# Kernel tuning notes

Hardware: AMD Instinct MI355X
Metric: run time of the kernel (lower is better)

## Reference

```python
import jax, jax.numpy as jnp
import numpy as np

D_MODEL = 1024
NUM_HEADS = 16
D_K = D_MODEL // NUM_HEADS


def setup_inputs() -> dict:
    key = jax.random.key(0)
    ks = jax.random.split(key, 11)
    B, S = 2, 2048
    scale = 1.0 / np.sqrt(D_MODEL)
    inp = {
        "q": jax.random.normal(ks[0], (B, S, D_MODEL), jnp.float32),
        "k": jax.random.normal(ks[1], (B, S, D_MODEL), jnp.float32),
        "v": jax.random.normal(ks[2], (B, S, D_MODEL), jnp.float32),
        "wq_w": jax.random.normal(ks[3], (D_MODEL, D_MODEL), jnp.float32) * scale,
        "wq_b": jnp.zeros((D_MODEL,), jnp.float32),
        "wk_w": jax.random.normal(ks[4], (D_MODEL, D_MODEL), jnp.float32) * scale,
        "wk_b": jnp.zeros((D_MODEL,), jnp.float32),
        "wv_w": jax.random.normal(ks[5], (D_MODEL, D_MODEL), jnp.float32) * scale,
        "wv_b": jnp.zeros((D_MODEL,), jnp.float32),
        "wo_w": jax.random.normal(ks[6], (D_MODEL, D_MODEL), jnp.float32) * scale,
        "wo_b": jnp.zeros((D_MODEL,), jnp.float32),
    }
    return inp


def reference(q, k, v, wq_w, wq_b, wk_w, wk_b, wv_w, wv_b, wo_w, wo_b):
    B, S, _ = q.shape
    H, dk = NUM_HEADS, D_K
    # projections (torch Linear: x @ W.T + b); reshape to [B, H, S, dk]
    qh = (q @ wq_w.T + wq_b).reshape(B, S, H, dk).transpose(0, 2, 1, 3)
    kh = (k @ wk_w.T + wk_b).reshape(B, S, H, dk).transpose(0, 2, 1, 3)
    vh = (v @ wv_w.T + wv_b).reshape(B, S, H, dk).transpose(0, 2, 1, 3)
    # explicit [B,H,S,S] scores, softmax over keys
    scores = jnp.einsum('bhqd,bhkd->bhqk', qh, kh) / np.sqrt(dk).astype(jnp.float32)
    weights = jax.nn.softmax(scores, axis=-1)
    out = jnp.einsum('bhqk,bhkd->bhqd', weights, vh)
    out = out.transpose(0, 2, 1, 3).reshape(B, S, H * dk)
    return out @ wo_w.T + wo_b
```

## Files before the change

kernel.cpp:

```cpp
#include <hip/hip_runtime.h>

#define B_  2
#define S_  2048
#define D_  1024
#define H_  16
#define DK_ 64

typedef __bf16 bf16;
typedef __bf16 bf16x8 __attribute__((ext_vector_type(8)));
typedef __bf16 bf16x4 __attribute__((ext_vector_type(4)));
typedef float  f32x4  __attribute__((ext_vector_type(4)));

#define GLD16(gptr, lptr) __builtin_amdgcn_global_load_lds( \
    (const __attribute__((address_space(1))) void*)(gptr),  \
    (__attribute__((address_space(3))) void*)(lptr), 16, 0, 0)

__global__ __launch_bounds__(256) void cast_all(
    const float* __restrict__ q, const float* __restrict__ k, const float* __restrict__ v,
    const float* __restrict__ wq, const float* __restrict__ wk, const float* __restrict__ wv,
    const float* __restrict__ wo,
    bf16* __restrict__ qb, bf16* __restrict__ kb, bf16* __restrict__ vb,
    bf16* __restrict__ wqb, bf16* __restrict__ wkb, bf16* __restrict__ wvb,
    bf16* __restrict__ wob) {
  int blk = blockIdx.x;
  const float* in; bf16* out; int base;
  if      (blk < 2048) { in = q;  out = qb;  base = blk; }
  else if (blk < 4096) { in = k;  out = kb;  base = blk - 2048; }
  else if (blk < 6144) { in = v;  out = vb;  base = blk - 4096; }
  else if (blk < 6656) { in = wq; out = wqb; base = blk - 6144; }
  else if (blk < 7168) { in = wk; out = wkb; base = blk - 6656; }
  else if (blk < 7680) { in = wv; out = wvb; base = blk - 7168; }
  else                 { in = wo; out = wob; base = blk - 7680; }
  int i = (base * 256 + threadIdx.x) * 8;
  float4 a = *(const float4*)(in + i);
  float4 b = *(const float4*)(in + i + 4);
  bf16x8 o;
  o[0] = (bf16)a.x; o[1] = (bf16)a.y; o[2] = (bf16)a.z; o[3] = (bf16)a.w;
  o[4] = (bf16)b.x; o[5] = (bf16)b.y; o[6] = (bf16)b.z; o[7] = (bf16)b.w;
  *(bf16x8*)(out + i) = o;
}

__global__ __launch_bounds__(256, 6) void gemm_qkv(
    const bf16* __restrict__ qb, const bf16* __restrict__ kb, const bf16* __restrict__ vb,
    const bf16* __restrict__ wq, const bf16* __restrict__ wk, const bf16* __restrict__ wv,
    const float* __restrict__ biq, const float* __restrict__ bik, const float* __restrict__ biv,
    bf16* __restrict__ Qh, bf16* __restrict__ Kh, bf16* __restrict__ Vt) {
  __shared__ bf16 As[128 * 64];
  __shared__ bf16 Bs[64 * 64];
  const int z = blockIdx.y;
  const bf16 *A, *Bm; const float* bias; bf16* Cout;
  int bx, by, N;
  if (z == 0)      { A = qb; Bm = wq; bias = biq; Cout = Qh; }
  else if (z == 1) { A = kb; Bm = wk; bias = bik; Cout = Kh; }
  else             { A = wv; Bm = vb; bias = biv; Cout = Vt; }
  if (z < 2) { by = blockIdx.x & 31; bx = blockIdx.x >> 5; N = D_; }
  else       { bx = blockIdx.x & 63; by = blockIdx.x >> 6; N = B_ * S_; }
  const int K = D_;

  const int tid  = threadIdx.x;
  const int wave = tid >> 6, lane = tid & 63;
  const int g = lane >> 4, r = lane & 15;
  const int m0 = by * 128, n0 = bx * 64;

  f32x4 acc[2][4] = {};
  const int srow = tid >> 3;
  const int sp   = tid & 7;

  for (int k0 = 0; k0 < K; k0 += 64) {
    __syncthreads();
#pragma unroll
    for (int rep = 0; rep < 4; rep++) {
      int row = rep * 32 + srow;
      int bb  = sp ^ (row & 7);
      GLD16(A + (size_t)(m0 + row) * K + k0 + bb * 8, As + rep * 2048 + wave * 512);
    }
#pragma unroll
    for (int rep = 0; rep < 2; rep++) {
      int row = rep * 32 + srow;
      int bb  = sp ^ (row & 7);
      GLD16(Bm + (size_t)(n0 + row) * K + k0 + bb * 8, Bs + rep * 2048 + wave * 512);
    }
    __syncthreads();

#pragma unroll
    for (int kc = 0; kc < 2; kc++) {
      bf16x8 af[2], bfr[4];
#pragma unroll
      for (int i = 0; i < 2; i++) {
        int row = wave * 32 + i * 16 + r;
        af[i] = *(const bf16x8*)(As + row * 64 + (((kc * 4 + g) ^ (row & 7)) * 8));
      }
#pragma unroll
      for (int j = 0; j < 4; j++) {
        int row = j * 16 + r;
        bfr[j] = *(const bf16x8*)(Bs + row * 64 + (((kc * 4 + g) ^ (row & 7)) * 8));
      }
#pragma unroll
      for (int i = 0; i < 2; i++)
#pragma unroll
        for (int j = 0; j < 4; j++)
          acc[i][j] = __builtin_amdgcn_mfma_f32_16x16x32_bf16(af[i], bfr[j], acc[i][j], 0, 0, 0);
    }
  }

  const float qscale = 0.18033688f;
#pragma unroll
  for (int i = 0; i < 2; i++) {
#pragma unroll
    for (int j = 0; j < 4; j++) {
#pragma unroll
      for (int t = 0; t < 4; t++) {
        int mrow = m0 + wave * 32 + i * 16 + g * 4 + t;
        int col  = n0 + j * 16 + r;
        float val = acc[i][j][t];
        if (z < 2) {
          val += bias[col];
          if (z == 0) val *= qscale;
          int bb2 = mrow >> 11, s = mrow & (S_ - 1);
          int hh = col >> 6, d = col & 63;
          Cout[(((size_t)(bb2 * H_ + hh)) * S_ + s) * 64 + d] = (bf16)val;
        } else {
          val += bias[mrow];
          Cout[(size_t)mrow * N + col] = (bf16)val;
        }
      }
    }
  }
}

__global__ __launch_bounds__(256, 6) void gemm_out(const bf16* __restrict__ A,
                                                   const bf16* __restrict__ Bm,
                                                   const float* __restrict__ bias,
                                                   float* __restrict__ Cout) {
  __shared__ bf16 As[128 * 64];
  __shared__ bf16 Bs[64 * 64];
  const int K = D_, N = D_;
  const int tid  = threadIdx.x;
  const int wave = tid >> 6, lane = tid & 63;
  const int g = lane >> 4, r = lane & 15;
  const int bx = blockIdx.x & 15, by = blockIdx.x >> 4;
  const int m0 = by * 128, n0 = bx * 64;

  f32x4 acc[2][4] = {};
  const int srow = tid >> 3;
  const int sp   = tid & 7;

  for (int k0 = 0; k0 < K; k0 += 64) {
    __syncthreads();
#pragma unroll
    for (int rep = 0; rep < 4; rep++) {
      int row = rep * 32 + srow;
      int bb  = sp ^ (row & 7);
      GLD16(A + (size_t)(m0 + row) * K + k0 + bb * 8, As + rep * 2048 + wave * 512);
    }
#pragma unroll
    for (int rep = 0; rep < 2; rep++) {
      int row = rep * 32 + srow;
      int bb  = sp ^ (row & 7);
      GLD16(Bm + (size_t)(n0 + row) * K + k0 + bb * 8, Bs + rep * 2048 + wave * 512);
    }
    __syncthreads();

#pragma unroll
    for (int kc = 0; kc < 2; kc++) {
      bf16x8 af[2], bfr[4];
#pragma unroll
      for (int i = 0; i < 2; i++) {
        int row = wave * 32 + i * 16 + r;
        af[i] = *(const bf16x8*)(As + row * 64 + (((kc * 4 + g) ^ (row & 7)) * 8));
      }
#pragma unroll
      for (int j = 0; j < 4; j++) {
        int row = j * 16 + r;
        bfr[j] = *(const bf16x8*)(Bs + row * 64 + (((kc * 4 + g) ^ (row & 7)) * 8));
      }
#pragma unroll
      for (int i = 0; i < 2; i++)
#pragma unroll
        for (int j = 0; j < 4; j++)
          acc[i][j] = __builtin_amdgcn_mfma_f32_16x16x32_bf16(af[i], bfr[j], acc[i][j], 0, 0, 0);
    }
  }

#pragma unroll
  for (int i = 0; i < 2; i++)
#pragma unroll
    for (int j = 0; j < 4; j++)
#pragma unroll
      for (int t = 0; t < 4; t++) {
        int mrow = m0 + wave * 32 + i * 16 + g * 4 + t;
        int col  = n0 + j * 16 + r;
        Cout[(size_t)mrow * N + col] = acc[i][j][t] + bias[col];
      }
}

__global__ __launch_bounds__(256, 4) void flash_attn(const bf16* __restrict__ Qh,
                                                     const bf16* __restrict__ Kh,
                                                     const bf16* __restrict__ Vt,
                                                     bf16* __restrict__ Apart,
                                                     float* __restrict__ Lpart) {
  __shared__ bf16 Ks[64 * 64];
  __shared__ bf16 Vs[64 * 64];
  __shared__ bf16 Ps[128 * 40];

  const int tid  = threadIdx.x;
  const int wave = tid >> 6, lane = tid & 63;
  const int g = lane >> 4, r = lane & 15;

  int qt = blockIdx.x >> 6;
  int kh = blockIdx.x & 1;
  int bh = (blockIdx.x >> 1) & 31;
  int h = bh & (H_ - 1), b = bh >> 4;

  const bf16* Kbase = Kh + ((size_t)bh * S_ + kh * 1024) * DK_;
  const bf16* Vbase = Vt + (size_t)h * 64 * (B_ * S_) + (size_t)b * S_ + kh * 1024;

  bf16x8 bq[2][2];
#pragma unroll
  for (int sq = 0; sq < 2; sq++) {
    int qrow = qt * 128 + wave * 32 + sq * 16 + r;
    const bf16* qp = Qh + ((size_t)bh * S_ + qrow) * DK_;
#pragma unroll
    for (int kc = 0; kc < 2; kc++)
      bq[sq][kc] = *(const bf16x8*)(qp + kc * 32 + g * 8);
  }

  f32x4 acc_o[2][4] = {};
  float l_run[2] = {0.f, 0.f};

  const int srow = tid >> 3, spp = tid & 7;

  for (int j0 = 0; j0 < 1024 / 64; j0++) {
    __syncthreads();
#pragma unroll
    for (int rep = 0; rep < 2; rep++) {
      int rr = rep * 32 + srow;
      int bb = spp ^ (rr & 7);
      GLD16(Kbase + (size_t)(j0 * 64 + rr) * 64 + bb * 8, Ks + rep * 2048 + wave * 512);
      GLD16(Vbase + (size_t)rr * (B_ * S_) + j0 * 64 + bb * 8, Vs + rep * 2048 + wave * 512);
    }
    __syncthreads();

    bf16x8 ak[4][2];
#pragma unroll
    for (int ks = 0; ks < 4; ks++) {
      int kr = ks * 16 + r;
#pragma unroll
      for (int kc = 0; kc < 2; kc++)
        ak[ks][kc] = *(const bf16x8*)(Ks + kr * 64 + (((kc * 4 + g) ^ (kr & 7)) * 8));
    }
    f32x4 sacc[2][4] = {};
#pragma unroll
    for (int sq = 0; sq < 2; sq++)
#pragma unroll
      for (int ks = 0; ks < 4; ks++)
#pragma unroll
        for (int kc = 0; kc < 2; kc++)
          sacc[sq][ks] = __builtin_amdgcn_mfma_f32_16x16x32_bf16(ak[ks][kc], bq[sq][kc],
                                                                 sacc[sq][ks], 0, 0, 0);

#pragma unroll
    for (int c = 0; c < 2; c++) {
#pragma unroll
      for (int sq = 0; sq < 2; sq++) {
        int qrow = wave * 32 + sq * 16 + r;
        float rs = 0.f;
#pragma unroll
        for (int k2 = 0; k2 < 2; k2++) {
          int ks = c * 2 + k2;
          bf16x4 pk;
#pragma unroll
          for (int t = 0; t < 4; t++) {
            float pv = __builtin_amdgcn_exp2f(sacc[sq][ks][t]);
            rs += pv;
            pk[t] = (bf16)pv;
          }
          *(bf16x4*)(Ps + qrow * 40 + k2 * 16 + g * 4) = pk;
        }
        l_run[sq] += rs;
      }
      asm volatile("s_waitcnt lgkmcnt(0)" ::: "memory");

      bf16x8 bp[2];
#pragma unroll
      for (int sq = 0; sq < 2; sq++) {
        int qrow = wave * 32 + sq * 16 + r;
        bp[sq] = *(const bf16x8*)(Ps + qrow * 40 + g * 8);
      }
#pragma unroll
      for (int dsub = 0; dsub < 4; dsub++) {
        int dr = dsub * 16 + r;
        bf16x8 av = *(const bf16x8*)(Vs + dr * 64 + (((c * 4 + g) ^ (dr & 7)) * 8));
#pragma unroll
        for (int sq = 0; sq < 2; sq++)
          acc_o[sq][dsub] = __builtin_amdgcn_mfma_f32_16x16x32_bf16(av, bp[sq],
                                                                    acc_o[sq][dsub], 0, 0, 0);
      }
    }
  }

#pragma unroll
  for (int sq = 0; sq < 2; sq++) {
    float l = l_run[sq];
    l += __shfl_xor(l, 16, 64);
    l += __shfl_xor(l, 32, 64);
    int s = qt * 128 + wave * 32 + sq * 16 + r;
    if (g == 0)
      Lpart[(size_t)kh * (B_ * H_ * S_) + (size_t)bh * S_ + s] = l;
    size_t base = (size_t)kh * (B_ * S_ * (size_t)D_) + ((size_t)b * S_ + s) * D_ + (size_t)h * 64;
#pragma unroll
    for (int dsub = 0; dsub < 4; dsub++) {
      bf16x4 o;
#pragma unroll
      for (int t = 0; t < 4; t++) o[t] = (bf16)(acc_o[sq][dsub][t]);
      *(bf16x4*)(Apart + base + dsub * 16 + g * 4) = o;
    }
  }
}

__global__ __launch_bounds__(256) void combine(const bf16* __restrict__ Apart,
                                               const float* __restrict__ Lpart,
                                               bf16* __restrict__ AO) {
  const size_t EQ = (size_t)B_ * S_ * D_;
  const int LHALF = B_ * H_ * S_;
  int idx = (blockIdx.x * 256 + threadIdx.x) * 8;
  int token = idx >> 10;
  int dcol  = idx & (D_ - 1);
  int b = token >> 11, s = token & (S_ - 1);
  int h = dcol >> 6;
  int li = (b * H_ + h) * S_ + s;
  float inv = 1.0f / (Lpart[li] + Lpart[li + LHALF]);
  bf16x8 a0 = *(const bf16x8*)(Apart + idx);
  bf16x8 a1 = *(const bf16x8*)(Apart + EQ + idx);
  bf16x8 o;
#pragma unroll
  for (int t = 0; t < 8; t++) o[t] = (bf16)(((float)a0[t] + (float)a1[t]) * inv);
  *(bf16x8*)(AO + idx) = o;
}

extern "C" void kernel_launch(void* const* d_in, const int* in_sizes, int n_in,
                              void* d_out, int out_size, void* d_ws, size_t ws_size,
                              hipStream_t stream) {
  const float* q    = (const float*)d_in[0];
  const float* k    = (const float*)d_in[1];
  const float* v    = (const float*)d_in[2];
  const float* wq_w = (const float*)d_in[3];
  const float* wq_b = (const float*)d_in[4];
  const float* wk_w = (const float*)d_in[5];
  const float* wk_b = (const float*)d_in[6];
  const float* wv_w = (const float*)d_in[7];
  const float* wv_b = (const float*)d_in[8];
  const float* wo_w = (const float*)d_in[9];
  const float* wo_b = (const float*)d_in[10];

  bf16* W = (bf16*)d_ws;
  const size_t NTOK = (size_t)B_ * S_;
  const size_t EQ = NTOK * D_;
  const size_t EW = (size_t)D_ * D_;
  bf16* qb  = W;
  bf16* kb  = qb  + EQ;
  bf16* vb  = kb  + EQ;
  bf16* Qhb = vb  + EQ;
  bf16* Khb = Qhb + EQ;
  bf16* Vtb = Khb + EQ;
  bf16* AOb = Vtb + EQ;
  bf16* wqb = AOb + EQ;
  bf16* wkb = wqb + EW;
  bf16* wvb = wkb + EW;
  bf16* wob = wvb + EW;

  bf16*  Apart = qb;
  float* Lpart = (float*)vb;

  cast_all<<<8192, 256, 0, stream>>>(q, k, v, wq_w, wk_w, wv_w, wo_w,
                                     qb, kb, vb, wqb, wkb, wvb, wob);

  gemm_qkv<<<dim3(512, 3), 256, 0, stream>>>(qb, kb, vb, wqb, wkb, wvb,
                                             wq_b, wk_b, wv_b, Qhb, Khb, Vtb);

  flash_attn<<<1024, 256, 0, stream>>>(Qhb, Khb, Vtb, Apart, Lpart);

  combine<<<2048, 256, 0, stream>>>(Apart, Lpart, AOb);

  gemm_out<<<512, 256, 0, stream>>>(AOb, wob, wo_b, (float*)d_out);
}
```

Measured before the change: 217.2 us.

## Double-buffer K/V tiles in flash attention and shrink P scratch

Adds a second LDS buffer for K and V so the next tile's global-to-LDS loads are issued before computing on the current tile, with explicit vmcnt waits and raw s_barrier instead of __syncthreads. The P staging buffer is halved by reusing one 16-row slot per wave for both query sub-tiles sequentially. It also wraps the MFMA sections in s_setprio and adds sched_barrier. This hides load latency behind compute but raises LDS use (about 37 KB per block), which may limit the 4-blocks-per-CU occupancy target and serializes the P write/read per sub-tile.

```diff
diff --git a/kernel.cpp b/kernel.cpp
--- a/kernel.cpp
+++ b/kernel.cpp
@@ -199,9 +199,9 @@
                                                      const bf16* __restrict__ Vt,
                                                      bf16* __restrict__ Apart,
                                                      float* __restrict__ Lpart) {
-  __shared__ bf16 Ks[64 * 64];
-  __shared__ bf16 Vs[64 * 64];
-  __shared__ bf16 Ps[128 * 40];
+  __shared__ bf16 Ks[2][64 * 64];
+  __shared__ bf16 Vs[2][64 * 64];
+  __shared__ bf16 Ps[64 * 40];
 
   const int tid  = threadIdx.x;
   const int wave = tid >> 6, lane = tid & 63;
@@ -230,16 +230,33 @@
 
   const int srow = tid >> 3, spp = tid & 7;
 
-  for (int j0 = 0; j0 < 1024 / 64; j0++) {
-    __syncthreads();
-#pragma unroll
-    for (int rep = 0; rep < 2; rep++) {
-      int rr = rep * 32 + srow;
-      int bb = spp ^ (rr & 7);
-      GLD16(Kbase + (size_t)(j0 * 64 + rr) * 64 + bb * 8, Ks + rep * 2048 + wave * 512);
-      GLD16(Vbase + (size_t)rr * (B_ * S_) + j0 * 64 + bb * 8, Vs + rep * 2048 + wave * 512);
-    }
-    __syncthreads();
+#define STAGE_KV(J, BUF) do {                                                        \
+    _Pragma("unroll")                                                                \
+    for (int rep = 0; rep < 2; rep++) {                                              \
+      int rr = rep * 32 + srow;                                                      \
+      int bb = spp ^ (rr & 7);                                                       \
+      GLD16(Kbase + (size_t)((J) * 64 + rr) * 64 + bb * 8,                           \
+            &Ks[BUF][rep * 2048 + wave * 512]);                                      \
+      GLD16(Vbase + (size_t)rr * (B_ * S_) + (J) * 64 + bb * 8,                      \
+            &Vs[BUF][rep * 2048 + wave * 512]);                                      \
+    }                                                                                \
+  } while (0)
+
+  STAGE_KV(0, 0);
+
+  for (int j0 = 0; j0 < 16; j0++) {
+    const int buf = j0 & 1;
+    __builtin_amdgcn_s_barrier();
+    if (j0 < 15) {
+      STAGE_KV(j0 + 1, buf ^ 1);
+      asm volatile("s_waitcnt vmcnt(4)" ::: "memory");
+    } else {
+      asm volatile("s_waitcnt vmcnt(0)" ::: "memory");
+    }
+    __builtin_amdgcn_s_barrier();
+
+    const bf16* KsB = Ks[buf];
+    const bf16* VsB = Vs[buf];
 
     bf16x8 ak[4][2];
 #pragma unroll
@@ -247,9 +264,10 @@
       int kr = ks * 16 + r;
 #pragma unroll
       for (int kc = 0; kc < 2; kc++)
-        ak[ks][kc] = *(const bf16x8*)(Ks + kr * 64 + (((kc * 4 + g) ^ (kr & 7)) * 8));
+        ak[ks][kc] = *(const bf16x8*)(KsB + kr * 64 + (((kc * 4 + g) ^ (kr & 7)) * 8));
     }
     f32x4 sacc[2][4] = {};
+    __builtin_amdgcn_s_setprio(1);
 #pragma unroll
     for (int sq = 0; sq < 2; sq++)
 #pragma unroll
@@ -258,12 +276,14 @@
         for (int kc = 0; kc < 2; kc++)
           sacc[sq][ks] = __builtin_amdgcn_mfma_f32_16x16x32_bf16(ak[ks][kc], bq[sq][kc],
                                                                  sacc[sq][ks], 0, 0, 0);
+    __builtin_amdgcn_s_setprio(0);
 
 #pragma unroll
     for (int c = 0; c < 2; c++) {
+      bf16x8 bp[2];
+      const int prow = wave * 16 + r;
 #pragma unroll
       for (int sq = 0; sq < 2; sq++) {
-        int qrow = wave * 32 + sq * 16 + r;
         float rs = 0.f;
 #pragma unroll
         for (int k2 = 0; k2 < 2; k2++) {
@@ -275,29 +295,27 @@
             rs += pv;
             pk[t] = (bf16)pv;
           }
-          *(bf16x4*)(Ps + qrow * 40 + k2 * 16 + g * 4) = pk;
+          *(bf16x4*)(Ps + prow * 40 + k2 * 16 + g * 4) = pk;
         }
         l_run[sq] += rs;
-      }
-      asm volatile("s_waitcnt lgkmcnt(0)" ::: "memory");
-
-      bf16x8 bp[2];
-#pragma unroll
-      for (int sq = 0; sq < 2; sq++) {
-        int qrow = wave * 32 + sq * 16 + r;
-        bp[sq] = *(const bf16x8*)(Ps + qrow * 40 + g * 8);
-      }
+        asm volatile("s_waitcnt lgkmcnt(0)" ::: "memory");
+        bp[sq] = *(const bf16x8*)(Ps + prow * 40 + g * 8);
+        __builtin_amdgcn_sched_barrier(0);
+      }
+      __builtin_amdgcn_s_setprio(1);
 #pragma unroll
       for (int dsub = 0; dsub < 4; dsub++) {
         int dr = dsub * 16 + r;
-        bf16x8 av = *(const bf16x8*)(Vs + dr * 64 + (((c * 4 + g) ^ (dr & 7)) * 8));
+        bf16x8 av = *(const bf16x8*)(VsB + dr * 64 + (((c * 4 + g) ^ (dr & 7)) * 8));
 #pragma unroll
         for (int sq = 0; sq < 2; sq++)
           acc_o[sq][dsub] = __builtin_amdgcn_mfma_f32_16x16x32_bf16(av, bp[sq],
                                                                     acc_o[sq][dsub], 0, 0, 0);
       }
-    }
-  }
+      __builtin_amdgcn_s_setprio(0);
+    }
+  }
+#undef STAGE_KV
 
 #pragma unroll
   for (int sq = 0; sq < 2; sq++) {
```

Result: slower. 226.6 us (+4.3%).

## Drop split-KV in flash attention and fuse normalization, removing combine kernel

Applied to the files above, without the earlier changes.

Each flash-attention block now processes the full 2048-key sequence for its query tile instead of half of it, and normalizes by the row sum directly before writing bf16 output. This removes the separate combine kernel, the partial-output and partial-sum writes and reads, and one launch. In exchange the grid halves to 512 blocks, which lowers parallelism on a GPU with 256 CUs and doubles the serial loop length per block. The softmax appears to use no running max, so dropping the split does not change the math.

```diff
diff --git a/kernel.cpp b/kernel.cpp
--- a/kernel.cpp
+++ b/kernel.cpp
@@ -197,8 +197,7 @@
 __global__ __launch_bounds__(256, 4) void flash_attn(const bf16* __restrict__ Qh,
                                                      const bf16* __restrict__ Kh,
                                                      const bf16* __restrict__ Vt,
-                                                     bf16* __restrict__ Apart,
-                                                     float* __restrict__ Lpart) {
+                                                     bf16* __restrict__ AO) {
   __shared__ bf16 Ks[64 * 64];
   __shared__ bf16 Vs[64 * 64];
   __shared__ bf16 Ps[128 * 40];
@@ -207,13 +206,12 @@
   const int wave = tid >> 6, lane = tid & 63;
   const int g = lane >> 4, r = lane & 15;
 
-  int qt = blockIdx.x >> 6;
-  int kh = blockIdx.x & 1;
-  int bh = (blockIdx.x >> 1) & 31;
+  int qt = blockIdx.x >> 5;
+  int bh = blockIdx.x & 31;
   int h = bh & (H_ - 1), b = bh >> 4;
 
-  const bf16* Kbase = Kh + ((size_t)bh * S_ + kh * 1024) * DK_;
-  const bf16* Vbase = Vt + (size_t)h * 64 * (B_ * S_) + (size_t)b * S_ + kh * 1024;
+  const bf16* Kbase = Kh + (size_t)bh * S_ * DK_;
+  const bf16* Vbase = Vt + (size_t)h * 64 * (B_ * S_) + (size_t)b * S_;
 
   bf16x8 bq[2][2];
 #pragma unroll
@@ -230,7 +228,7 @@
 
   const int srow = tid >> 3, spp = tid & 7;
 
-  for (int j0 = 0; j0 < 1024 / 64; j0++) {
+  for (int j0 = 0; j0 < S_ / 64; j0++) {
     __syncthreads();
 #pragma unroll
     for (int rep = 0; rep < 2; rep++) {
@@ -304,38 +302,17 @@
     float l = l_run[sq];
     l += __shfl_xor(l, 16, 64);
     l += __shfl_xor(l, 32, 64);
+    float inv = 1.0f / l;
     int s = qt * 128 + wave * 32 + sq * 16 + r;
-    if (g == 0)
-      Lpart[(size_t)kh * (B_ * H_ * S_) + (size_t)bh * S_ + s] = l;
-    size_t base = (size_t)kh * (B_ * S_ * (size_t)D_) + ((size_t)b * S_ + s) * D_ + (size_t)h * 64;
+    size_t base = ((size_t)b * S_ + s) * D_ + (size_t)h * 64;
 #pragma unroll
     for (int dsub = 0; dsub < 4; dsub++) {
       bf16x4 o;
 #pragma unroll
-      for (int t = 0; t < 4; t++) o[t] = (bf16)(acc_o[sq][dsub][t]);
-      *(bf16x4*)(Apart + base + dsub * 16 + g * 4) = o;
-    }
-  }
-}
-
-__global__ __launch_bounds__(256) void combine(const bf16* __restrict__ Apart,
-                                               const float* __restrict__ Lpart,
-                                               bf16* __restrict__ AO) {
-  const size_t EQ = (size_t)B_ * S_ * D_;
-  const int LHALF = B_ * H_ * S_;
-  int idx = (blockIdx.x * 256 + threadIdx.x) * 8;
-  int token = idx >> 10;
-  int dcol  = idx & (D_ - 1);
-  int b = token >> 11, s = token & (S_ - 1);
-  int h = dcol >> 6;
-  int li = (b * H_ + h) * S_ + s;
-  float inv = 1.0f / (Lpart[li] + Lpart[li + LHALF]);
-  bf16x8 a0 = *(const bf16x8*)(Apart + idx);
-  bf16x8 a1 = *(const bf16x8*)(Apart + EQ + idx);
-  bf16x8 o;
-#pragma unroll
-  for (int t = 0; t < 8; t++) o[t] = (bf16)(((float)a0[t] + (float)a1[t]) * inv);
-  *(bf16x8*)(AO + idx) = o;
+      for (int t = 0; t < 4; t++) o[t] = (bf16)(acc_o[sq][dsub][t] * inv);
+      *(bf16x4*)(AO + base + dsub * 16 + g * 4) = o;
+    }
+  }
 }
 
 extern "C" void kernel_launch(void* const* d_in, const int* in_sizes, int n_in,
@@ -369,18 +346,13 @@
   bf16* wvb = wkb + EW;
   bf16* wob = wvb + EW;
 
-  bf16*  Apart = qb;
-  float* Lpart = (float*)vb;
-
   cast_all<<<8192, 256, 0, stream>>>(q, k, v, wq_w, wk_w, wv_w, wo_w,
                                      qb, kb, vb, wqb, wkb, wvb, wob);
 
   gemm_qkv<<<dim3(512, 3), 256, 0, stream>>>(qb, kb, vb, wqb, wkb, wvb,
                                              wq_b, wk_b, wv_b, Qhb, Khb, Vtb);
 
-  flash_attn<<<1024, 256, 0, stream>>>(Qhb, Khb, Vtb, Apart, Lpart);
-
-  combine<<<2048, 256, 0, stream>>>(Apart, Lpart, AOb);
+  flash_attn<<<512, 256, 0, stream>>>(Qhb, Khb, Vtb, AOb);
 
   gemm_out<<<512, 256, 0, stream>>>(AOb, wob, wo_b, (float*)d_out);
 }
```

Result: no change. 220.4 us (+1.5%).
